# Performance work log

Measured on AMD Instinct MI355X. Metric: run time of the kernel, lower is better.

Reference implementation:

```python
import jax, jax.numpy as jnp
import numpy as np

B = 2097152  # batch
H = 2        # GRU hidden size


def _gru_cell(x, h, w_ih, w_hh, b_ih, b_hh):
    # torch.nn.GRUCell math. w_ih: [3H, I], w_hh: [3H, H]
    gi = x @ w_ih.T + b_ih  # [B, 3H]
    gh = h @ w_hh.T + b_hh  # [B, 3H]
    i_r, i_z, i_n = jnp.split(gi, 3, axis=-1)
    h_r, h_z, h_n = jnp.split(gh, 3, axis=-1)
    r = jax.nn.sigmoid(i_r + h_r)
    z = jax.nn.sigmoid(i_z + h_z)
    n = jnp.tanh(i_n + r * h_n)
    return (1.0 - z) * n + z * h


def setup_inputs() -> dict:
    key = jax.random.key(0)
    ks = jax.random.split(key, 14)
    f32 = jnp.float32
    inp = {
        "x": jax.random.normal(ks[0], (B, 18), dtype=f32),
        # r_up: GRUCell(2, 2)
        "w_ih_up": 0.3 * jax.random.normal(ks[1], (3 * H, 2), dtype=f32),
        "w_hh_up": 0.3 * jax.random.normal(ks[2], (3 * H, H), dtype=f32),
        "b_ih_up": 0.1 * jax.random.normal(ks[3], (3 * H,), dtype=f32),
        "b_hh_up": 0.1 * jax.random.normal(ks[4], (3 * H,), dtype=f32),
        # fc_obs: Linear(6, 2)
        "w_obs": 0.3 * jax.random.normal(ks[5], (2, 6), dtype=f32),
        "b_obs": 0.1 * jax.random.normal(ks[6], (2,), dtype=f32),
        # r_down: GRUCell(2, 2)
        "w_ih_dn": 0.3 * jax.random.normal(ks[7], (3 * H, 2), dtype=f32),
        "w_hh_dn": 0.3 * jax.random.normal(ks[8], (3 * H, H), dtype=f32),
        "b_ih_dn": 0.1 * jax.random.normal(ks[9], (3 * H,), dtype=f32),
        "b_hh_dn": 0.1 * jax.random.normal(ks[10], (3 * H,), dtype=f32),
        # fc_out: Linear(2, 1)
        "w_out": 0.3 * jax.random.normal(ks[11], (1, H), dtype=f32),
        "b_out": 0.1 * jax.random.normal(ks[12], (1,), dtype=f32),
    }
    return inp


def reference(x, w_ih_up, w_hh_up, b_ih_up, b_hh_up, w_obs, b_obs,
              w_ih_dn, w_hh_dn, b_ih_dn, b_hh_dn, w_out, b_out):
    obs = x[:, :4]            # [B, 4]
    j = x[:, 4:11]            # [B, 7]
    jd = x[:, 11:]            # [B, 7]
    jcat = jnp.stack([j, jd], axis=1)  # [B, 2, 7]

    # upward recurrence over the 7 joints, reversed order
    h = jnp.zeros((x.shape[0], H), dtype=x.dtype)
    h_up = []
    for i in reversed(range(7)):
        h = _gru_cell(jcat[:, :, i], h, w_ih_up, w_hh_up, b_ih_up, b_hh_up)
        h_up.append(h)

    # fuse observation into the hidden state
    h = jnp.concatenate([obs, h], axis=1) @ w_obs.T + b_obs  # [B, 2]

    # downward recurrence, emitting one action per joint
    acts = []
    for i in range(7):
        h = _gru_cell(h_up[i], h, w_ih_dn, w_hh_dn, b_ih_dn, b_hh_dn)
        acts.append(h @ w_out.T + b_out)  # [B, 1]
    return jnp.concatenate(acts, axis=1)  # [B, 7]
```

## Files before the change

kernel.cpp:

```cpp
#include <hip/hip_runtime.h>


using v2f = __attribute__((ext_vector_type(2))) float;

__device__ __forceinline__ float fexp2(float x) { return __builtin_amdgcn_exp2f(x); }
__device__ __forceinline__ float frcp(float x)  { return __builtin_amdgcn_rcpf(x); }

struct Cell {
    v2f wr0, wr1, ur0, ur1, br;
    v2f wz0, wz1, uz0, uz1, bz;
    v2f wn0, wn1, bni;
    v2f un0, un1, bnh;
};

__device__ __forceinline__ Cell make_cell(const float* __restrict__ wi,
                                          const float* __restrict__ wh,
                                          const float* __restrict__ bi,
                                          const float* __restrict__ bh) {
    const float s1 = -1.4426950408889634f;
    const float s2 =  2.8853900817779268f;
    Cell c;
    c.wr0 = (v2f){s1*wi[0], s1*wi[2]};  c.wr1 = (v2f){s1*wi[1], s1*wi[3]};
    c.ur0 = (v2f){s1*wh[0], s1*wh[2]};  c.ur1 = (v2f){s1*wh[1], s1*wh[3]};
    c.br  = (v2f){s1*(bi[0]+bh[0]), s1*(bi[1]+bh[1])};
    c.wz0 = (v2f){s1*wi[4], s1*wi[6]};  c.wz1 = (v2f){s1*wi[5], s1*wi[7]};
    c.uz0 = (v2f){s1*wh[4], s1*wh[6]};  c.uz1 = (v2f){s1*wh[5], s1*wh[7]};
    c.bz  = (v2f){s1*(bi[2]+bh[2]), s1*(bi[3]+bh[3])};
    c.wn0 = (v2f){s2*wi[8], s2*wi[10]}; c.wn1 = (v2f){s2*wi[9], s2*wi[11]};
    c.bni = (v2f){s2*bi[4], s2*bi[5]};
    c.un0 = (v2f){s2*wh[8], s2*wh[10]}; c.un1 = (v2f){s2*wh[9], s2*wh[11]};
    c.bnh = (v2f){s2*bh[4], s2*bh[5]};
    return c;
}

__device__ __forceinline__ void gru(const Cell& c, float x0, float x1, v2f& h) {
    v2f gr = c.br + c.wr0 * x0 + c.wr1 * x1 + c.ur0 * h.x + c.ur1 * h.y;
    v2f gz = c.bz + c.wz0 * x0 + c.wz1 * x1 + c.uz0 * h.x + c.uz1 * h.y;
    v2f r  = (v2f){ frcp(1.0f + fexp2(gr.x)), frcp(1.0f + fexp2(gr.y)) };
    v2f z  = (v2f){ frcp(1.0f + fexp2(gz.x)), frcp(1.0f + fexp2(gz.y)) };
    v2f in = c.bni + c.wn0 * x0 + c.wn1 * x1;
    v2f hn = c.bnh + c.un0 * h.x + c.un1 * h.y;
    v2f a  = in + r * hn;
    v2f n  = (v2f){ 1.0f - 2.0f * frcp(1.0f + fexp2(a.x)),
                    1.0f - 2.0f * frcp(1.0f + fexp2(a.y)) };
    h = n + z * (h - n);
}

__global__ __launch_bounds__(256) void recpolicy_kernel(
    const float* __restrict__ x,
    const float* __restrict__ w_ih_up, const float* __restrict__ w_hh_up,
    const float* __restrict__ b_ih_up, const float* __restrict__ b_hh_up,
    const float* __restrict__ w_obs,   const float* __restrict__ b_obs,
    const float* __restrict__ w_ih_dn, const float* __restrict__ w_hh_dn,
    const float* __restrict__ b_ih_dn, const float* __restrict__ b_hh_dn,
    const float* __restrict__ w_out,   const float* __restrict__ b_out,
    float* __restrict__ out, int n)
{
    __shared__ float lds[4608];
    const int tid  = threadIdx.x;
    const int row0 = blockIdx.x * 256;
    const int rows = min(256, n - row0);

    if (rows == 256) {
        const float4* src = reinterpret_cast<const float4*>(x + (size_t)row0 * 18);
        float4* dst = reinterpret_cast<float4*>(lds);
        #pragma unroll
        for (int i = 0; i < 5; ++i) {
            int idx = tid + i * 256;
            if (idx < 1152) dst[idx] = src[idx];
        }
    } else {
        for (int idx = tid; idx < rows * 18; idx += 256)
            lds[idx] = x[(size_t)row0 * 18 + idx];
    }
    __syncthreads();

    float xv[18];
    {
        const float2* r2 = reinterpret_cast<const float2*>(lds + tid * 18);
        #pragma unroll
        for (int i = 0; i < 9; ++i) { float2 v = r2[i]; xv[2*i] = v.x; xv[2*i+1] = v.y; }
    }
    __syncthreads();

    Cell up = make_cell(w_ih_up, w_hh_up, b_ih_up, b_hh_up);
    v2f h = (v2f){0.0f, 0.0f};
    v2f hu[7];
    #pragma unroll
    for (int k = 0; k < 7; ++k) {
        const int i = 6 - k;
        gru(up, xv[4 + i], xv[11 + i], h);
        hu[k] = h;
    }

    {
        v2f t = (v2f){b_obs[0], b_obs[1]};
        #pragma unroll
        for (int c = 0; c < 4; ++c)
            t += (v2f){w_obs[c], w_obs[6 + c]} * xv[c];
        t += (v2f){w_obs[4], w_obs[10]} * h.x;
        t += (v2f){w_obs[5], w_obs[11]} * h.y;
        h = t;
    }

    Cell dn = make_cell(w_ih_dn, w_hh_dn, b_ih_dn, b_hh_dn);
    const float wo0 = w_out[0], wo1 = w_out[1], bo = b_out[0];
    #pragma unroll
    for (int k = 0; k < 7; ++k) {
        gru(dn, hu[k].x, hu[k].y, h);
        lds[tid * 7 + k] = wo0 * h.x + wo1 * h.y + bo;
    }
    __syncthreads();

    if (rows == 256) {
        float4* dst = reinterpret_cast<float4*>(out + (size_t)row0 * 7);
        const float4* src = reinterpret_cast<const float4*>(lds);
        #pragma unroll
        for (int i = 0; i < 2; ++i) {
            int idx = tid + i * 256;
            if (idx < 448) dst[idx] = src[idx];
        }
    } else {
        for (int idx = tid; idx < rows * 7; idx += 256)
            out[(size_t)row0 * 7 + idx] = lds[idx];
    }
}

extern "C" void kernel_launch(void* const* d_in, const int* in_sizes, int n_in,
                              void* d_out, int out_size, void* d_ws, size_t ws_size,
                              hipStream_t stream) {
    const float* x       = (const float*)d_in[0];
    const float* w_ih_up = (const float*)d_in[1];
    const float* w_hh_up = (const float*)d_in[2];
    const float* b_ih_up = (const float*)d_in[3];
    const float* b_hh_up = (const float*)d_in[4];
    const float* w_obs   = (const float*)d_in[5];
    const float* b_obs   = (const float*)d_in[6];
    const float* w_ih_dn = (const float*)d_in[7];
    const float* w_hh_dn = (const float*)d_in[8];
    const float* b_ih_dn = (const float*)d_in[9];
    const float* b_hh_dn = (const float*)d_in[10];
    const float* w_out   = (const float*)d_in[11];
    const float* b_out   = (const float*)d_in[12];
    float* out = (float*)d_out;

    const int n = in_sizes[0] / 18;
    const int block = 256;
    const int grid = (n + block - 1) / block;
    recpolicy_kernel<<<grid, block, 0, stream>>>(
        x, w_ih_up, w_hh_up, b_ih_up, b_hh_up, w_obs, b_obs,
        w_ih_dn, w_hh_dn, b_ih_dn, b_hh_dn, w_out, b_out, out, n);
}
```

Measured before the change: 52.94 us.

## Use scalar GRU math with shared reciprocals and tighter launch bounds

Drops the packed v2f pre-scaled weight struct and computes each GRU gate in scalar form, reading weights straight from the (uniform) pointers. Sigmoid and tanh pairs now share a single reciprocal of the product of their denominators, which halves the rcp count but adds multiplies. Each thread reads its input row lazily from LDS instead of loading all 18 values into registers. Launch bounds now request 6 waves per SIMD to cut register pressure. The exp scaling multiply moves into the activation, and the shared reciprocal can overflow when both denominators are large.

```diff
diff --git a/kernel.cpp b/kernel.cpp
--- a/kernel.cpp
+++ b/kernel.cpp
@@ -1,52 +1,50 @@
 #include <hip/hip_runtime.h>
 
-
-using v2f = __attribute__((ext_vector_type(2))) float;
 
 __device__ __forceinline__ float fexp2(float x) { return __builtin_amdgcn_exp2f(x); }
 __device__ __forceinline__ float frcp(float x)  { return __builtin_amdgcn_rcpf(x); }
 
-struct Cell {
-    v2f wr0, wr1, ur0, ur1, br;
-    v2f wz0, wz1, uz0, uz1, bz;
-    v2f wn0, wn1, bni;
-    v2f un0, un1, bnh;
-};
+#define S1n (-1.4426950408889634f)
+#define S2p ( 2.8853900817779268f)
 
-__device__ __forceinline__ Cell make_cell(const float* __restrict__ wi,
-                                          const float* __restrict__ wh,
-                                          const float* __restrict__ bi,
-                                          const float* __restrict__ bh) {
-    const float s1 = -1.4426950408889634f;
-    const float s2 =  2.8853900817779268f;
-    Cell c;
-    c.wr0 = (v2f){s1*wi[0], s1*wi[2]};  c.wr1 = (v2f){s1*wi[1], s1*wi[3]};
-    c.ur0 = (v2f){s1*wh[0], s1*wh[2]};  c.ur1 = (v2f){s1*wh[1], s1*wh[3]};
-    c.br  = (v2f){s1*(bi[0]+bh[0]), s1*(bi[1]+bh[1])};
-    c.wz0 = (v2f){s1*wi[4], s1*wi[6]};  c.wz1 = (v2f){s1*wi[5], s1*wi[7]};
-    c.uz0 = (v2f){s1*wh[4], s1*wh[6]};  c.uz1 = (v2f){s1*wh[5], s1*wh[7]};
-    c.bz  = (v2f){s1*(bi[2]+bh[2]), s1*(bi[3]+bh[3])};
-    c.wn0 = (v2f){s2*wi[8], s2*wi[10]}; c.wn1 = (v2f){s2*wi[9], s2*wi[11]};
-    c.bni = (v2f){s2*bi[4], s2*bi[5]};
-    c.un0 = (v2f){s2*wh[8], s2*wh[10]}; c.un1 = (v2f){s2*wh[9], s2*wh[11]};
-    c.bnh = (v2f){s2*bh[4], s2*bh[5]};
-    return c;
+__device__ __forceinline__ void sigmoid2(float g0, float g1, float& r0, float& r1) {
+    float d0 = 1.0f + fexp2(S1n * g0);
+    float d1 = 1.0f + fexp2(S1n * g1);
+    float inv = frcp(d0 * d1);
+    r0 = inv * d1;
+    r1 = inv * d0;
+}
+__device__ __forceinline__ void tanh2(float a0, float a1, float& n0, float& n1) {
+    float d0 = 1.0f + fexp2(S2p * a0);
+    float d1 = 1.0f + fexp2(S2p * a1);
+    float m = -2.0f * frcp(d0 * d1);
+    n0 = fmaf(m, d1, 1.0f);
+    n1 = fmaf(m, d0, 1.0f);
 }
 
-__device__ __forceinline__ void gru(const Cell& c, float x0, float x1, v2f& h) {
-    v2f gr = c.br + c.wr0 * x0 + c.wr1 * x1 + c.ur0 * h.x + c.ur1 * h.y;
-    v2f gz = c.bz + c.wz0 * x0 + c.wz1 * x1 + c.uz0 * h.x + c.uz1 * h.y;
-    v2f r  = (v2f){ frcp(1.0f + fexp2(gr.x)), frcp(1.0f + fexp2(gr.y)) };
-    v2f z  = (v2f){ frcp(1.0f + fexp2(gz.x)), frcp(1.0f + fexp2(gz.y)) };
-    v2f in = c.bni + c.wn0 * x0 + c.wn1 * x1;
-    v2f hn = c.bnh + c.un0 * h.x + c.un1 * h.y;
-    v2f a  = in + r * hn;
-    v2f n  = (v2f){ 1.0f - 2.0f * frcp(1.0f + fexp2(a.x)),
-                    1.0f - 2.0f * frcp(1.0f + fexp2(a.y)) };
-    h = n + z * (h - n);
+__device__ __forceinline__ void gru_cell(
+    const float* __restrict__ wi, const float* __restrict__ wh,
+    const float* __restrict__ bi, const float* __restrict__ bh,
+    float x0, float x1, float& h0, float& h1)
+{
+    float g0 = (bi[0] + bh[0]) + wi[0]*x0 + wi[1]*x1 + wh[0]*h0 + wh[1]*h1;
+    float g1 = (bi[1] + bh[1]) + wi[2]*x0 + wi[3]*x1 + wh[2]*h0 + wh[3]*h1;
+    float g2 = (bi[2] + bh[2]) + wi[4]*x0 + wi[5]*x1 + wh[4]*h0 + wh[5]*h1;
+    float g3 = (bi[3] + bh[3]) + wi[6]*x0 + wi[7]*x1 + wh[6]*h0 + wh[7]*h1;
+    float r0, r1, z0, z1;
+    sigmoid2(g0, g1, r0, r1);
+    sigmoid2(g2, g3, z0, z1);
+    float in0 = bi[4] + wi[8]*x0  + wi[9]*x1;
+    float in1 = bi[5] + wi[10]*x0 + wi[11]*x1;
+    float hn0 = bh[4] + wh[8]*h0  + wh[9]*h1;
+    float hn1 = bh[5] + wh[10]*h0 + wh[11]*h1;
+    float n0, n1;
+    tanh2(in0 + r0 * hn0, in1 + r1 * hn1, n0, n1);
+    h0 = n0 + z0 * (h0 - n0);
+    h1 = n1 + z1 * (h1 - n1);
 }
 
-__global__ __launch_bounds__(256) void recpolicy_kernel(
+__global__ __launch_bounds__(256, 6) void recpolicy_kernel(
     const float* __restrict__ x,
     const float* __restrict__ w_ih_up, const float* __restrict__ w_hh_up,
     const float* __restrict__ b_ih_up, const float* __restrict__ b_hh_up,
@@ -75,40 +73,36 @@
     }
     __syncthreads();
 
-    float xv[18];
+    const float* myrow = lds + tid * 18;
+
+    float h0 = 0.0f, h1 = 0.0f;
+    float hu0[7], hu1[7];
+    #pragma unroll
+    for (int k = 0; k < 7; ++k) {
+        const int i = 6 - k;
+        float xj  = myrow[4 + i];
+        float xjd = myrow[11 + i];
+        gru_cell(w_ih_up, w_hh_up, b_ih_up, b_hh_up, xj, xjd, h0, h1);
+        hu0[k] = h0;
+        hu1[k] = h1;
+    }
+
     {
-        const float2* r2 = reinterpret_cast<const float2*>(lds + tid * 18);
-        #pragma unroll
-        for (int i = 0; i < 9; ++i) { float2 v = r2[i]; xv[2*i] = v.x; xv[2*i+1] = v.y; }
+        float o0 = myrow[0], o1 = myrow[1], o2 = myrow[2], o3 = myrow[3];
+        float t0 = b_obs[0] + w_obs[0]*o0 + w_obs[1]*o1 + w_obs[2]*o2 + w_obs[3]*o3
+                 + w_obs[4]*h0 + w_obs[5]*h1;
+        float t1 = b_obs[1] + w_obs[6]*o0 + w_obs[7]*o1 + w_obs[8]*o2 + w_obs[9]*o3
+                 + w_obs[10]*h0 + w_obs[11]*h1;
+        h0 = t0;
+        h1 = t1;
     }
     __syncthreads();
 
-    Cell up = make_cell(w_ih_up, w_hh_up, b_ih_up, b_hh_up);
-    v2f h = (v2f){0.0f, 0.0f};
-    v2f hu[7];
-    #pragma unroll
-    for (int k = 0; k < 7; ++k) {
-        const int i = 6 - k;
-        gru(up, xv[4 + i], xv[11 + i], h);
-        hu[k] = h;
-    }
-
-    {
-        v2f t = (v2f){b_obs[0], b_obs[1]};
-        #pragma unroll
-        for (int c = 0; c < 4; ++c)
-            t += (v2f){w_obs[c], w_obs[6 + c]} * xv[c];
-        t += (v2f){w_obs[4], w_obs[10]} * h.x;
-        t += (v2f){w_obs[5], w_obs[11]} * h.y;
-        h = t;
-    }
-
-    Cell dn = make_cell(w_ih_dn, w_hh_dn, b_ih_dn, b_hh_dn);
     const float wo0 = w_out[0], wo1 = w_out[1], bo = b_out[0];
     #pragma unroll
     for (int k = 0; k < 7; ++k) {
-        gru(dn, hu[k].x, hu[k].y, h);
-        lds[tid * 7 + k] = wo0 * h.x + wo1 * h.y + bo;
+        gru_cell(w_ih_dn, w_hh_dn, b_ih_dn, b_hh_dn, hu0[k], hu1[k], h0, h1);
+        lds[tid * 7 + k] = fmaf(wo0, h0, fmaf(wo1, h1, bo));
     }
     __syncthreads();
 
```

New measurement: 68.21 us. 28.8% more time.
